# Kernel tuning notes

Hardware: AMD Instinct MI355X
Metric: run time of the kernel (lower is better)

The kernel has to match this reference:

```python
import jax, jax.numpy as jnp
import numpy as np

# WFLW 98-point curve decomposition: (start, end) landmark index ranges (end exclusive)
CURVES = [(0, 33), (33, 42), (42, 51), (51, 60), (60, 68), (68, 76), (76, 88), (88, 98)]
SIGMA_W2 = [15.0] * len(CURVES)  # get_sigmaV2(...)/4, constant per curve
N_PT = 98
LEFT_EYE, RIGHT_EYE = 60, 72  # eye-corner indices for the 98-point branch


def curve_loss(p, g, sigma_w2):
    # p, g: [B, n, 2] landmarks of one facial curve
    c_p = (p[:, :-1] + p[:, 1:]) * 0.5   # segment centers, [B, n-1, 2]
    tau_p = p[:, 1:] - p[:, :-1]          # segment tangents, [B, n-1, 2]
    c_g = (g[:, :-1] + g[:, 1:]) * 0.5
    tau_g = g[:, 1:] - g[:, :-1]
    c = jnp.concatenate([c_p, c_g], axis=1)        # [B, M, 2], M = 2*(n-1)
    tau = jnp.concatenate([tau_p, -tau_g], axis=1)  # [B, M, 2]
    # pairwise RBF kernel on segment centers: exp(-||c_i - c_j||^2 / sigma)
    d2 = jnp.sum((c[:, :, None, :] - c[:, None, :, :]) ** 2, axis=-1)  # [B, M, M]
    weight = jnp.exp(-d2 / sigma_w2)
    dot = jnp.einsum('bid,bjd->bij', tau, tau)  # pairwise tangent dot products
    return jnp.sum(weight * dot, axis=(1, 2))   # [B]


def reference(pred, gt):
    batch = pred.shape[0]
    pl = pred.reshape(batch, -1, 2)  # [B, 98, 2]
    gl = gt.reshape(batch, -1, 2)
    mean_error = jnp.mean(jnp.linalg.norm(pl - gl, axis=-1), axis=-1)  # [B]
    eye_dist = jnp.linalg.norm(gl[:, LEFT_EYE] - gl[:, RIGHT_EYE], axis=-1)  # [B]
    landmark_error = jnp.mean(mean_error / eye_dist)
    curve_error = jnp.zeros((batch,), dtype=pred.dtype)
    for (a, b), s2 in zip(CURVES, SIGMA_W2):
        curve_error = curve_error + curve_loss(pl[:, a:b], gl[:, a:b], s2)
    curve_error = jnp.mean(curve_error / (N_PT * eye_dist))
    return 0.8 * landmark_error + 0.2 * curve_error


def setup_inputs() -> dict:
    key = jax.random.key(0)
    k1, k2 = jax.random.split(key)
    pred = jax.random.normal(k1, (16384, 196), dtype=jnp.float32)
    gt = jax.random.normal(k2, (16384, 196), dtype=jnp.float32)
    return {"pred": pred, "gt": gt}
```

## Files before the change

### kernel.cpp

```cpp
#include <hip/hip_runtime.h>
#include <math.h>

static constexpr int NPT = 98;
static constexpr float CSCALE_HALF = 0.155064240f;

#if __has_builtin(__builtin_amdgcn_exp2f)
#define EXP2F(x) __builtin_amdgcn_exp2f(x)
#else
#define EXP2F(x) exp2f(x)
#endif
#if __has_builtin(__builtin_amdgcn_sqrtf)
#define SQRTF(x) __builtin_amdgcn_sqrtf(x)
#else
#define SQRTF(x) sqrtf(x)
#endif

typedef float v2f __attribute__((ext_vector_type(2)));
typedef float v4a __attribute__((ext_vector_type(4)));
typedef float v4fu __attribute__((ext_vector_type(4), aligned(8)));
typedef _Float16 h2 __attribute__((ext_vector_type(2)));
typedef _Float16 h4 __attribute__((ext_vector_type(4)));

#if __has_builtin(__builtin_amdgcn_fdot2)
#define FDOT2(a, b, c) __builtin_amdgcn_fdot2((a), (b), (c), false)
#else
#define FDOT2(a, b, c) fmaf((float)(a).x, (float)(b).x, fmaf((float)(a).y, (float)(b).y, (c)))
#endif

#if __has_builtin(__builtin_amdgcn_cvt_pkrtz)
#define PKRTZ(x, y) __builtin_bit_cast(h2, __builtin_amdgcn_cvt_pkrtz((x), (y)))
#else
static __device__ __forceinline__ h2 PKRTZ(float x, float y) {
    h2 r; r.x = (_Float16)x; r.y = (_Float16)y; return r;
}
#endif


__device__ __forceinline__ float wdt(h4 si, h4 sj) {
    h2 dc = si.xy - sj.xy;
    float d2 = FDOT2(dc, dc, 0.0f);
    float dt = FDOT2(si.zw, sj.zw, 0.0f);
    return EXP2F(-d2) * dt;
}

__global__ __launch_bounds__(256, 8)
void lddmm_main(const float* __restrict__ pred, const float* __restrict__ gt,
                float* __restrict__ ws) {
    __shared__ h4 sh[4][256];
    const int wave = threadIdx.x >> 6;
    const int lane = threadIdx.x & 63;
    const int b = blockIdx.x * 4 + wave;

    const float* pf = pred + (size_t)b * (2 * NPT);
    const float* gf = gt + (size_t)b * (2 * NPT);
    const v2f* g2 = (const v2f*)gf;
    h4* sw = sh[wave];

    v2f e0 = g2[60];
    v2f e1 = g2[72];

    float diag = 0.0f;
    float accS = 0.0f;
    float accA = 0.0f;
    float accB = 0.0f;
    float dsum = 0.0f;

    #pragma unroll
    for (int pass = 0; pass < 3; ++pass) {
        int s = lane + 64 * pass;
        if (s < 180) {
            int A, NS, B, rel;
            if (s < 64)       { A = 0;  NS = 32; B = 0;   rel = s; }
            else if (s < 80)  { A = 33; NS = 8;  B = 96;  rel = s - 64; }
            else if (s < 96)  { A = 42; NS = 8;  B = 118; rel = s - 80; }
            else if (s < 112) { A = 51; NS = 8;  B = 140; rel = s - 96; }
            else if (s < 126) { A = 60; NS = 7;  B = 162; rel = s - 112; }
            else if (s < 140) { A = 68; NS = 7;  B = 182; rel = s - 126; }
            else if (s < 162) { A = 76; NS = 11; B = 202; rel = s - 140; }
            else              { A = 88; NS = 9;  B = 230; rel = s - 162; }
            bool isg = rel >= NS;
            int a = A + (isg ? rel - NS : rel);
            const float* src = isg ? gf : pf;
            v4fu q = *(const v4fu*)(src + 2 * a);
            v2f c = (q.xy + q.zw) * CSCALE_HALF;
            v2f tau = q.zw - q.xy;
            if (isg) tau = -tau;
            diag = fmaf(tau.x, tau.x, diag);
            diag = fmaf(tau.y, tau.y, diag);
            h2 ch = PKRTZ(c.x, c.y);
            h2 th = PKRTZ(tau.x, tau.y);
            h4 v; v.x = ch.x; v.y = ch.y; v.z = th.x; v.w = th.y;
            sw[B + rel] = v;
            int DUPN = (B == 0) ? 32 : 6;
            if (rel < DUPN) sw[B + 2 * NS + rel] = v;
        }
    }

    if (lane < 49) {
        v4a p4 = *(const v4a*)(pf + 4 * lane);
        v4a g4 = *(const v4a*)(gf + 4 * lane);
        v2f d0 = p4.xy - g4.xy;
        v2f d1 = p4.zw - g4.zw;
        dsum = SQRTF(d0.x * d0.x + d0.y * d0.y) + SQRTF(d1.x * d1.x + d1.y * d1.y);
    }

    asm volatile("s_waitcnt lgkmcnt(0)" ::: "memory");

    {
        h4 sjA = sw[lane];
        h4 sjB = sw[lane + 32];
        #pragma unroll 4
        for (int t = 1; t <= 15; ++t) {
            h4 r = sw[lane + t];
            accA += wdt(r, sjA);
            accB += wdt(r, sjB);
        }
        { h4 r = sw[lane + 16]; accA += wdt(r, sjA); }
        accS += wdt(sjA, sjB);
    }

    {
        int base, jl, h, TA, TB; float mm;
        if      (lane < 8)  { base = 96;  jl = lane;      h = 8;  TA = 4; TB = 3; mm = 1.f; }
        else if (lane < 16) { base = 118; jl = lane - 8;  h = 8;  TA = 4; TB = 3; mm = 1.f; }
        else if (lane < 24) { base = 140; jl = lane - 16; h = 8;  TA = 4; TB = 3; mm = 1.f; }
        else if (lane < 31) { base = 162; jl = lane - 24; h = 7;  TA = 3; TB = 3; mm = 1.f; }
        else if (lane < 38) { base = 182; jl = lane - 31; h = 7;  TA = 3; TB = 3; mm = 1.f; }
        else if (lane < 49) { base = 202; jl = lane - 38; h = 11; TA = 5; TB = 5; mm = 1.f; }
        else if (lane < 58) { base = 230; jl = lane - 49; h = 9;  TA = 4; TB = 4; mm = 1.f; }
        else                { base = 202; jl = 0;         h = 11; TA = 0; TB = 0; mm = 0.f; }
        const h4* sp = sw + base + jl;
        h4 sjA = sp[0];
        h4 sjB = sp[h];
        accA = fmaf(mm, wdt(sjA, sjB), accA);
        #pragma unroll
        for (int t = 1; t <= 5; ++t) {
            h4 u1 = sp[t];
            h4 u2 = sp[h + t];
            float mA = (t <= TA) ? 1.0f : 0.0f;
            float mB = (t <= TB) ? 1.0f : 0.0f;
            accA = fmaf(mA, wdt(u1, sjA) + wdt(u2, sjB), accA);
            accB = fmaf(mB, wdt(u1, sjB) + wdt(u2, sjA), accB);
        }
    }

    float v = 0.8f * dsum + 0.2f * (fmaf(2.0f, accA + accB, diag + accS));
    #pragma unroll
    for (int off = 32; off >= 1; off >>= 1) v += __shfl_xor(v, off, 64);

    if (lane == 0) {
        v2f de = e0 - e1;
        float eye = SQRTF(de.x * de.x + de.y * de.y);
        ws[b] = v / ((float)NPT * eye);
    }
}

__global__ __launch_bounds__(1024)
void lddmm_reduce(const float* __restrict__ ws, float* __restrict__ out,
                  int n4, float invbatch) {
    __shared__ float sm[1024];
    const int t = threadIdx.x;
    const float4* w4 = (const float4*)ws;
    float s = 0.0f;
    for (int i = t; i < n4; i += 1024) {
        float4 v = w4[i];
        s += (v.x + v.y) + (v.z + v.w);
    }
    sm[t] = s;
    __syncthreads();
    for (int off = 512; off >= 1; off >>= 1) {
        if (t < off) sm[t] += sm[t + off];
        __syncthreads();
    }
    if (t == 0) out[0] = sm[0] * invbatch;
}

extern "C" void kernel_launch(void* const* d_in, const int* in_sizes, int n_in,
                              void* d_out, int out_size, void* d_ws, size_t ws_size,
                              hipStream_t stream) {
    const float* pred = (const float*)d_in[0];
    const float* gt = (const float*)d_in[1];
    float* out = (float*)d_out;
    float* ws = (float*)d_ws;
    const int batch = in_sizes[0] / (2 * NPT);

    lddmm_main<<<batch / 4, 256, 0, stream>>>(pred, gt, ws);
    lddmm_reduce<<<1, 1024, 0, stream>>>(ws, out, batch / 4, 1.0f / (float)batch);
}
```

Baseline: 26.38 us.

## Stage landmarks in LDS and fuse final reduction via last-block atomic counter

```diff
diff --git a/kernel.cpp b/kernel.cpp
--- a/kernel.cpp
+++ b/kernel.cpp
@@ -17,7 +17,6 @@
 
 typedef float v2f __attribute__((ext_vector_type(2)));
 typedef float v4a __attribute__((ext_vector_type(4)));
-typedef float v4fu __attribute__((ext_vector_type(4), aligned(8)));
 typedef _Float16 h2 __attribute__((ext_vector_type(2)));
 typedef _Float16 h4 __attribute__((ext_vector_type(4)));
 
@@ -45,16 +44,23 @@
 
 __global__ __launch_bounds__(256, 8)
 void lddmm_main(const float* __restrict__ pred, const float* __restrict__ gt,
-                float* __restrict__ ws) {
+                float* __restrict__ ws, int* __restrict__ cnt,
+                float* __restrict__ out, float invbatch) {
+    __shared__ alignas(16) v2f Pp[4][100];
+    __shared__ alignas(16) v2f Pg[4][100];
     __shared__ h4 sh[4][256];
-    const int wave = threadIdx.x >> 6;
-    const int lane = threadIdx.x & 63;
+    __shared__ float part[4];
+    __shared__ float red[256];
+    __shared__ int isLast;
+    const int tid = threadIdx.x;
+    const int wave = tid >> 6;
+    const int lane = tid & 63;
     const int b = blockIdx.x * 4 + wave;
+    h4* sw = sh[wave];
 
     const float* pf = pred + (size_t)b * (2 * NPT);
     const float* gf = gt + (size_t)b * (2 * NPT);
     const v2f* g2 = (const v2f*)gf;
-    h4* sw = sh[wave];
 
     v2f e0 = g2[60];
     v2f e1 = g2[72];
@@ -64,6 +70,18 @@
     float accA = 0.0f;
     float accB = 0.0f;
     float dsum = 0.0f;
+
+    if (lane < 49) {
+        v4a p4 = *(const v4a*)(pf + 4 * lane);
+        v4a g4 = *(const v4a*)(gf + 4 * lane);
+        v2f d0 = p4.xy - g4.xy;
+        v2f d1 = p4.zw - g4.zw;
+        dsum = SQRTF(d0.x * d0.x + d0.y * d0.y)
+             + SQRTF(d1.x * d1.x + d1.y * d1.y);
+        *(v4a*)&Pp[wave][2 * lane] = p4;
+        *(v4a*)&Pg[wave][2 * lane] = g4;
+    }
+    asm volatile("s_waitcnt lgkmcnt(0)" ::: "memory");
 
     #pragma unroll
     for (int pass = 0; pass < 3; ++pass) {
@@ -80,10 +98,11 @@
             else              { A = 88; NS = 9;  B = 230; rel = s - 162; }
             bool isg = rel >= NS;
             int a = A + (isg ? rel - NS : rel);
-            const float* src = isg ? gf : pf;
-            v4fu q = *(const v4fu*)(src + 2 * a);
-            v2f c = (q.xy + q.zw) * CSCALE_HALF;
-            v2f tau = q.zw - q.xy;
+            const v2f* arr = isg ? Pg[wave] : Pp[wave];
+            v2f q0 = arr[a];
+            v2f q1 = arr[a + 1];
+            v2f c = (q0 + q1) * CSCALE_HALF;
+            v2f tau = q1 - q0;
             if (isg) tau = -tau;
             diag = fmaf(tau.x, tau.x, diag);
             diag = fmaf(tau.y, tau.y, diag);
@@ -95,15 +114,6 @@
             if (rel < DUPN) sw[B + 2 * NS + rel] = v;
         }
     }
-
-    if (lane < 49) {
-        v4a p4 = *(const v4a*)(pf + 4 * lane);
-        v4a g4 = *(const v4a*)(gf + 4 * lane);
-        v2f d0 = p4.xy - g4.xy;
-        v2f d1 = p4.zw - g4.zw;
-        dsum = SQRTF(d0.x * d0.x + d0.y * d0.y) + SQRTF(d1.x * d1.x + d1.y * d1.y);
-    }
-
     asm volatile("s_waitcnt lgkmcnt(0)" ::: "memory");
 
     {
@@ -144,35 +154,42 @@
         }
     }
 
-    float v = 0.8f * dsum + 0.2f * (fmaf(2.0f, accA + accB, diag + accS));
+    float v = 0.8f * dsum + 0.2f * fmaf(2.0f, accA + accB, diag + accS);
     #pragma unroll
     for (int off = 32; off >= 1; off >>= 1) v += __shfl_xor(v, off, 64);
 
     if (lane == 0) {
         v2f de = e0 - e1;
         float eye = SQRTF(de.x * de.x + de.y * de.y);
-        ws[b] = v / ((float)NPT * eye);
-    }
-}
-
-__global__ __launch_bounds__(1024)
-void lddmm_reduce(const float* __restrict__ ws, float* __restrict__ out,
-                  int n4, float invbatch) {
-    __shared__ float sm[1024];
-    const int t = threadIdx.x;
-    const float4* w4 = (const float4*)ws;
-    float s = 0.0f;
-    for (int i = t; i < n4; i += 1024) {
-        float4 v = w4[i];
-        s += (v.x + v.y) + (v.z + v.w);
-    }
-    sm[t] = s;
+        part[wave] = v / ((float)NPT * eye);
+    }
     __syncthreads();
-    for (int off = 512; off >= 1; off >>= 1) {
-        if (t < off) sm[t] += sm[t + off];
+
+    if (tid == 0) {
+        ws[blockIdx.x] = (part[0] + part[1]) + (part[2] + part[3]);
+        __threadfence();
+        int old = atomicAdd(cnt, 1);
+        isLast = (old == (int)gridDim.x - 1);
+    }
+    __syncthreads();
+    if (isLast) {
+        __threadfence();
+        const float4* w4 = (const float4*)ws;
+        const int n4 = (int)gridDim.x / 4;
+        float s = 0.0f;
+        for (int i = tid; i < n4; i += 256) {
+            float4 q = w4[i];
+            s += (q.x + q.y) + (q.z + q.w);
+        }
+        red[tid] = s;
         __syncthreads();
-    }
-    if (t == 0) out[0] = sm[0] * invbatch;
+        #pragma unroll
+        for (int off = 128; off >= 1; off >>= 1) {
+            if (tid < off) red[tid] += red[tid + off];
+            __syncthreads();
+        }
+        if (tid == 0) out[0] = red[0] * invbatch;
+    }
 }
 
 extern "C" void kernel_launch(void* const* d_in, const int* in_sizes, int n_in,
@@ -183,7 +200,10 @@
     float* out = (float*)d_out;
     float* ws = (float*)d_ws;
     const int batch = in_sizes[0] / (2 * NPT);
-
-    lddmm_main<<<batch / 4, 256, 0, stream>>>(pred, gt, ws);
-    lddmm_reduce<<<1, 1024, 0, stream>>>(ws, out, batch / 4, 1.0f / (float)batch);
-}
+    const int nblk = batch / 4;
+
+    int* cnt = (int*)((char*)d_ws + (size_t)nblk * sizeof(float));
+    hipMemsetAsync(cnt, 0, sizeof(int), stream);
+    lddmm_main<<<nblk, 256, 0, stream>>>(pred, gt, ws, cnt, out,
+                                         1.0f / (float)batch);
+}
```

Result: slower. 93.77 us (+255.5%).
